# Performance work log

Measured on AMD Instinct MI355X. Metric: run time of the kernel, lower is better.

## Reference

```python
import jax, jax.numpy as jnp
import numpy as np

LN_EPS = 1e-5  # torch LayerNorm default
EPSILON = 1e-8  # slot attention epsilon


def layer_norm(x, g, b):
    mu = jnp.mean(x, axis=-1, keepdims=True)
    var = jnp.var(x, axis=-1, keepdims=True)
    return (x - mu) * jax.lax.rsqrt(var + LN_EPS) * g + b


def setup_inputs() -> dict:
    key = jax.random.key(0)
    ks = jax.random.split(key, 12)
    B, N, S, D, M = 64, 4096, 8, 256, 1024
    s = 0.02
    return {
        "features": jax.random.normal(ks[0], (B, N, D), jnp.float32),
        "slots_init": jax.random.normal(ks[1], (B, S, D), jnp.float32),
        # LayerNorm params (feature, slots, mlp)
        "g_feat": jnp.ones((D,), jnp.float32), "b_feat": jnp.zeros((D,), jnp.float32),
        "g_slots": jnp.ones((D,), jnp.float32), "b_slots": jnp.zeros((D,), jnp.float32),
        "g_mlp": jnp.ones((D,), jnp.float32), "b_mlp": jnp.zeros((D,), jnp.float32),
        # k/v/q projections (torch Linear weight: [out,in], no bias)
        "Wk": jax.random.normal(ks[2], (D, D), jnp.float32) * s,
        "Wv": jax.random.normal(ks[3], (D, D), jnp.float32) * s,
        "Wq": jax.random.normal(ks[4], (D, D), jnp.float32) * s,
        # GRUCell params: weight_ih/hh [3D, D] (gate order r, z, n), biases [3D]
        "w_ih": jax.random.normal(ks[5], (3 * D, D), jnp.float32) * s,
        "w_hh": jax.random.normal(ks[6], (3 * D, D), jnp.float32) * s,
        "b_ih": jnp.zeros((3 * D,), jnp.float32),
        "b_hh": jnp.zeros((3 * D,), jnp.float32),
        # MLP: Linear(D->M), ReLU, Linear(M->D)
        "W1": jax.random.normal(ks[7], (M, D), jnp.float32) * s,
        "b1": jnp.zeros((M,), jnp.float32),
        "W2": jax.random.normal(ks[8], (D, M), jnp.float32) * s,
        "b2": jnp.zeros((D,), jnp.float32),
        "num_iter": 3,
    }


def gru_cell(x, h, w_ih, w_hh, b_ih, b_hh):
    # x, h: [B*, D]; torch.nn.GRUCell math, gate order r, z, n
    gi = x @ w_ih.T + b_ih  # [B*, 3D]
    gh = h @ w_hh.T + b_hh
    i_r, i_z, i_n = jnp.split(gi, 3, axis=-1)
    h_r, h_z, h_n = jnp.split(gh, 3, axis=-1)
    r = jax.nn.sigmoid(i_r + h_r)
    z = jax.nn.sigmoid(i_z + h_z)
    n = jnp.tanh(i_n + r * h_n)
    return (1.0 - z) * n + z * h


def reference(features, slots_init, g_feat, b_feat, g_slots, b_slots, g_mlp, b_mlp,
              Wk, Wv, Wq, w_ih, w_hh, b_ih, b_hh, W1, b1, W2, b2, num_iter):
    feats = layer_norm(features, g_feat, b_feat)          # [B, N, D]
    k = feats @ Wk.T                                      # [B, N, D]
    v = feats @ Wv.T                                      # [B, N, D]
    B, N, D = v.shape
    scale = D ** -0.5
    slots = slots_init                                    # [B, S, D]
    S = slots.shape[1]
    attn = None
    for _ in range(num_iter):
        slots_prev = slots
        q = layer_norm(slots, g_slots, b_slots) @ Wq.T    # [B, S, D]
        attn_logits = jnp.einsum('bid,bjd->bij', q, k) * scale  # [B, S, N]
        attn = jax.nn.softmax(attn_logits, axis=1)        # softmax over slots
        attn = attn + EPSILON
        attn_wm = attn / jnp.sum(attn, axis=-1, keepdims=True)
        updates = jnp.einsum('bij,bjd->bid', attn_wm, v)  # [B, S, D]
        slots = gru_cell(updates.reshape(-1, D), slots_prev.reshape(-1, D),
                         w_ih, w_hh, b_ih, b_hh).reshape(B, S, D)
        h = jax.nn.relu(layer_norm(slots, g_mlp, b_mlp) @ W1.T + b1)
        slots = slots + h @ W2.T + b2
    return slots, attn
```

## Files before the change

### kernel.cpp

```cpp
#include <hip/hip_runtime.h>
#include <stdint.h>

typedef unsigned short u16;
typedef unsigned int u32;
typedef __bf16 bf16_t;
typedef bf16_t bf16x8 __attribute__((ext_vector_type(8)));
typedef float f32x4 __attribute__((ext_vector_type(4)));

#define DEV static __device__ __forceinline__

DEV float bf2f(u16 a) {
  union { u32 u; float f; } c; c.u = ((u32)a) << 16; return c.f;
}
DEV u16 f2bf(float f) {
  union { float f; u32 u; } c; c.f = f;
  return (u16)((c.u + 0x7FFFu + ((c.u >> 16) & 1u)) >> 16);
}
DEV f32x4 mfma16(bf16x8 a, bf16x8 b, f32x4 c) {
  return __builtin_amdgcn_mfma_f32_16x16x32_bf16(a, b, c, 0, 0, 0);
}
DEV float wave_sum(float v) {
#pragma unroll
  for (int off = 32; off > 0; off >>= 1) v += __shfl_xor(v, off, 64);
  return v;
}
DEV float sum16(float v) {
  v += __shfl_xor(v, 1, 64);
  v += __shfl_xor(v, 2, 64);
  v += __shfl_xor(v, 4, 64);
  v += __shfl_xor(v, 8, 64);
  return v;
}

__global__ void __launch_bounds__(256) init_prep(
    const float* __restrict__ Wk, const float* __restrict__ Wv,
    const float* __restrict__ gfeat, const float* __restrict__ bfeat,
    const float* __restrict__ slots_init,
    const float* __restrict__ Wq, const float* __restrict__ w_ih,
    const float* __restrict__ w_hh, const float* __restrict__ W1,
    const float* __restrict__ W2,
    u16* __restrict__ wkvp, float* __restrict__ ckv, float* __restrict__ dkv,
    float* __restrict__ slots,
    u16* __restrict__ wqb, u16* __restrict__ wihb, u16* __restrict__ whhb,
    u16* __restrict__ w1b, u16* __restrict__ w2b) {
  const int blk = blockIdx.x;
  const int tid = threadIdx.x;
  if (blk < 128) {
    const int o = blk * 4 + (tid >> 6);
    const int lane = tid & 63;
    const int d = lane * 4;
    const float* wrow = (o < 256) ? (Wk + (size_t)o * 256) : (Wv + (size_t)(o - 256) * 256);
    float4 w4 = *(const float4*)(wrow + d);
    float4 g4 = *(const float4*)(gfeat + d);
    float4 b4 = *(const float4*)(bfeat + d);
    float w[4] = {w4.x, w4.y, w4.z, w4.w};
    float g[4] = {g4.x, g4.y, g4.z, g4.w};
    float b[4] = {b4.x, b4.y, b4.z, b4.w};
    float cs = 0.f, ds = 0.f;
    u16 outp[4];
#pragma unroll
    for (int j = 0; j < 4; j++) {
      float wg = w[j] * g[j];
      cs += wg;
      ds += b[j] * w[j];
      outp[j] = f2bf(wg);
    }
    *(ushort4*)(wkvp + (size_t)o * 256 + d) = make_ushort4(outp[0], outp[1], outp[2], outp[3]);
    cs = wave_sum(cs);
    ds = wave_sum(ds);
    if (lane == 0) { ckv[o] = cs; dkv[o] = ds; }
  } else if (blk < 256) {
    const int idx = (blk - 128) * 1024 + tid * 4;
    *(float4*)(slots + idx) = *(const float4*)(slots_init + idx);
  } else {
    const int i = (blk - 256) * 1024 + tid * 4;
    const float* src; u16* dst; int off;
    if (i < 65536)       { src = Wq;   dst = wqb;  off = i; }
    else if (i < 262144) { src = w_ih; dst = wihb; off = i - 65536; }
    else if (i < 458752) { src = w_hh; dst = whhb; off = i - 262144; }
    else if (i < 720896) { src = W1;   dst = w1b;  off = i - 458752; }
    else                 { src = W2;   dst = w2b;  off = i - 720896; }
    float4 v = *(const float4*)(src + off);
    *(ushort4*)(dst + off) = make_ushort4(f2bf(v.x), f2bf(v.y), f2bf(v.z), f2bf(v.w));
  }
}

__global__ void __launch_bounds__(256, 2) gemm_kv(
    const float* __restrict__ feat, const u16* __restrict__ wkvp,
    const float* __restrict__ ckv, const float* __restrict__ dkv,
    u16* __restrict__ kbuf, u16* __restrict__ vtbuf) {
  __shared__ u16 Asm[128 * 256];
  __shared__ float mus[128];
  __shared__ float rss[128];
  const int tid = threadIdx.x;
  const int lane = tid & 63;
  const int wv = tid >> 6;
  const int cl = lane & 15;
  const int rq = lane >> 4;
  const int M0 = blockIdx.x * 128;
  const int wm = (wv & 1) * 64;
  const int wn = (wv >> 1) * 64;

#pragma unroll 4
  for (int i = 0; i < 16; i++) {
    const int gr = i * 256 + tid;
    const int m = gr >> 5;
    const int kc = gr & 31;
    const float* fp = feat + (size_t)(M0 + m) * 256 + kc * 8;
    float4 a0 = *(const float4*)fp;
    float4 a1 = *(const float4*)(fp + 4);
    float t1 = a0.x + a0.y + a0.z + a0.w + a1.x + a1.y + a1.z + a1.w;
    float t2 = a0.x * a0.x + a0.y * a0.y + a0.z * a0.z + a0.w * a0.w +
               a1.x * a1.x + a1.y * a1.y + a1.z * a1.z + a1.w * a1.w;
    t1 += __shfl_xor(t1, 1, 64);  t2 += __shfl_xor(t2, 1, 64);
    t1 += __shfl_xor(t1, 2, 64);  t2 += __shfl_xor(t2, 2, 64);
    t1 += __shfl_xor(t1, 4, 64);  t2 += __shfl_xor(t2, 4, 64);
    t1 += __shfl_xor(t1, 8, 64);  t2 += __shfl_xor(t2, 8, 64);
    t1 += __shfl_xor(t1, 16, 64); t2 += __shfl_xor(t2, 16, 64);
    if ((lane & 31) == 0) {
      float mu = t1 * (1.f / 256.f);
      float var = t2 * (1.f / 256.f) - mu * mu;
      mus[m] = mu;
      rss[m] = rsqrtf(var + 1e-5f);
    }
    u32 p0 = (u32)f2bf(a0.x) | ((u32)f2bf(a0.y) << 16);
    u32 p1 = (u32)f2bf(a0.z) | ((u32)f2bf(a0.w) << 16);
    u32 p2 = (u32)f2bf(a1.x) | ((u32)f2bf(a1.y) << 16);
    u32 p3 = (u32)f2bf(a1.z) | ((u32)f2bf(a1.w) << 16);
    const int sw = (kc & 24) | ((kc & 7) ^ (m & 7));
    *(uint4*)&Asm[m * 256 + sw * 8] = make_uint4(p0, p1, p2, p3);
  }
  __syncthreads();

  const f32x4 Z = {0.f, 0.f, 0.f, 0.f};
  const int b = M0 >> 12;
  const int col = cl;
  const int rq4 = rq * 4;

  for (int oc = 0; oc < 4; oc++) {
    const int O0 = oc * 128;
    f32x4 acc[4][4];
#pragma unroll
    for (int i = 0; i < 4; i++)
#pragma unroll
      for (int j = 0; j < 4; j++) acc[i][j] = Z;

#pragma unroll 2
    for (int kc8 = 0; kc8 < 8; kc8++) {
      bf16x8 af[4], bfr[4];
      const int c = kc8 * 4 + rq;
#pragma unroll
      for (int t = 0; t < 4; t++) {
        const int m = wm + t * 16 + cl;
        const int ca = (c & 24) | ((c & 7) ^ (m & 7));
        af[t] = *(const bf16x8*)&Asm[m * 256 + ca * 8];
        const int o = O0 + wn + t * 16 + cl;
        bfr[t] = *(const bf16x8*)(wkvp + (size_t)o * 256 + kc8 * 32 + rq * 8);
      }
#pragma unroll
      for (int i = 0; i < 4; i++)
#pragma unroll
        for (int j = 0; j < 4; j++) acc[i][j] = mfma16(af[i], bfr[j], acc[i][j]);
    }

    if (O0 < 256) {
#pragma unroll
      for (int i = 0; i < 4; i++) {
        const int mb = M0 + wm + i * 16 + rq4;
        const int ml = wm + i * 16 + rq4;
        float mu0[4], rs0[4];
#pragma unroll
        for (int r = 0; r < 4; r++) { mu0[r] = mus[ml + r]; rs0[r] = rss[ml + r]; }
#pragma unroll
        for (int j = 0; j < 4; j++) {
          const int o = O0 + wn + j * 16 + col;
          const float ck = ckv[o], dk = dkv[o];
#pragma unroll
          for (int r = 0; r < 4; r++) {
            float val = rs0[r] * acc[i][j][r] - rs0[r] * mu0[r] * ck + dk;
            kbuf[(size_t)(mb + r) * 256 + o] = f2bf(val);
          }
        }
      }
    } else {
#pragma unroll
      for (int i = 0; i < 4; i++) {
        const int mb = M0 + wm + i * 16 + rq4;
        const int ml = wm + i * 16 + rq4;
        const int n = mb & 4095;
        float mu0[4], rs0[4];
#pragma unroll
        for (int r = 0; r < 4; r++) { mu0[r] = mus[ml + r]; rs0[r] = rss[ml + r]; }
#pragma unroll
        for (int j = 0; j < 4; j++) {
          const int ov = O0 - 256 + wn + j * 16 + col;
          const float ck = ckv[ov + 256], dk = dkv[ov + 256];
          u16 t0 = f2bf(rs0[0] * acc[i][j][0] - rs0[0] * mu0[0] * ck + dk);
          u16 t1 = f2bf(rs0[1] * acc[i][j][1] - rs0[1] * mu0[1] * ck + dk);
          u16 t2 = f2bf(rs0[2] * acc[i][j][2] - rs0[2] * mu0[2] * ck + dk);
          u16 t3 = f2bf(rs0[3] * acc[i][j][3] - rs0[3] * mu0[3] * ck + dk);
          *(ushort4*)(vtbuf + (size_t)(b * 256 + ov) * 4096 + n) = make_ushort4(t0, t1, t2, t3);
        }
      }
    }
  }
}

__global__ void __launch_bounds__(256) attn_pass(
    const float* __restrict__ slots, const float* __restrict__ gs, const float* __restrict__ bs,
    const u16* __restrict__ wqb,
    const u16* __restrict__ kbuf, const u16* __restrict__ vtbuf,
    float* __restrict__ part_acc, float* __restrict__ part_den,
    float* __restrict__ attn_out, int store_attn) {
  __shared__ u16 pt[16 * 264];
  __shared__ u16 qld[16 * 264];
  const int chunk = blockIdx.x;
  const int b = blockIdx.y;
  const int n0 = chunk * 256;
  const int tid = threadIdx.x;
  const int lane = tid & 63;
  const int wv = tid >> 6;
  const int cl = lane & 15;
  const int rq = lane >> 4;
  const f32x4 Z = {0.f, 0.f, 0.f, 0.f};

  for (int i = tid; i < 8 * 264; i += 256) pt[8 * 264 + i] = 0;
  for (int rr = 0; rr < 2; rr++) {
    const int s = wv * 2 + rr;
    float4 x4 = *(const float4*)(slots + ((size_t)b * 8 + s) * 256 + lane * 4);
    float x[4] = {x4.x, x4.y, x4.z, x4.w};
    float s1 = x[0] + x[1] + x[2] + x[3];
    float s2 = x[0] * x[0] + x[1] * x[1] + x[2] * x[2] + x[3] * x[3];
    s1 = wave_sum(s1);
    s2 = wave_sum(s2);
    float mu = s1 * (1.f / 256.f);
    float rstd = rsqrtf(s2 * (1.f / 256.f) - mu * mu + 1e-5f);
    float4 g4 = *(const float4*)(gs + lane * 4);
    float4 b4 = *(const float4*)(bs + lane * 4);
    u16 o4[4];
    o4[0] = f2bf((x[0] - mu) * rstd * g4.x + b4.x);
    o4[1] = f2bf((x[1] - mu) * rstd * g4.y + b4.y);
    o4[2] = f2bf((x[2] - mu) * rstd * g4.z + b4.z);
    o4[3] = f2bf((x[3] - mu) * rstd * g4.w + b4.w);
    *(ushort4*)&pt[s * 264 + lane * 4] = make_ushort4(o4[0], o4[1], o4[2], o4[3]);
  }
  __syncthreads();

  {
    bf16x8 af[8];
#pragma unroll
    for (int ks = 0; ks < 8; ks++)
      af[ks] = *(const bf16x8*)&pt[cl * 264 + ks * 32 + rq * 8];
#pragma unroll
    for (int t = 0; t < 4; t++) {
      const int of = wv * 64 + t * 16;
      f32x4 acc = Z;
#pragma unroll
      for (int ks = 0; ks < 8; ks++) {
        bf16x8 bw = *(const bf16x8*)(wqb + (size_t)(of + cl) * 256 + ks * 32 + rq * 8);
        acc = mfma16(af[ks], bw, acc);
      }
#pragma unroll
      for (int r = 0; r < 4; r++)
        qld[(rq * 4 + r) * 264 + of + cl] = f2bf(acc[r]);
    }
  }
  __syncthreads();

  bf16x8 aq[8];
#pragma unroll
  for (int ks = 0; ks < 8; ks++)
    aq[ks] = *(const bf16x8*)&qld[cl * 264 + ks * 32 + rq * 8];

  float dacc[4] = {0.f, 0.f, 0.f, 0.f};
#pragma unroll
  for (int t = 0; t < 4; t++) {
    const int nl = (wv * 4 + t) * 16;
    f32x4 acc = Z;
    const int n = n0 + nl + cl;
#pragma unroll
    for (int ks = 0; ks < 8; ks++) {
      bf16x8 bk = *(const bf16x8*)(kbuf + ((size_t)b * 4096 + n) * 256 + ks * 32 + rq * 8);
      acc = mfma16(aq[ks], bk, acc);
    }
    float l[4];
#pragma unroll
    for (int r = 0; r < 4; r++) l[r] = acc[r] * 0.0625f;
    float m4 = fmaxf(fmaxf(l[0], l[1]), fmaxf(l[2], l[3]));
    float m8 = fmaxf(m4, __shfl_xor(m4, 16, 64));
    float e[4];
    float s4 = 0.f;
#pragma unroll
    for (int r = 0; r < 4; r++) { e[r] = __expf(l[r] - m8); s4 += e[r]; }
    float s8 = s4 + __shfl_xor(s4, 16, 64);
    float inv = 1.f / s8;
    float pa[4];
#pragma unroll
    for (int r = 0; r < 4; r++) pa[r] = e[r] * inv + 1e-8f;
#pragma unroll
    for (int r = 0; r < 4; r++) pt[(rq * 4 + r) * 264 + nl + cl] = f2bf(pa[r]);
    if (store_attn && lane < 32) {
#pragma unroll
      for (int r = 0; r < 4; r++)
        attn_out[((size_t)b * 8 + rq * 4 + r) * 4096 + n0 + nl + cl] = pa[r];
    }
#pragma unroll
    for (int r = 0; r < 4; r++) dacc[r] += sum16(pa[r]);
  }
  if (cl == 0 && lane < 32) {
#pragma unroll
    for (int r = 0; r < 4; r++)
      part_den[(((size_t)b * 16 + chunk) * 4 + wv) * 8 + rq * 4 + r] = dacc[r];
  }
  __syncthreads();

  bf16x8 ap[8];
#pragma unroll
  for (int ks = 0; ks < 8; ks++)
    ap[ks] = *(const bf16x8*)&pt[cl * 264 + ks * 32 + rq * 8];
#pragma unroll
  for (int t = 0; t < 4; t++) {
    const int df = wv * 64 + t * 16;
    f32x4 acc = Z;
    const int d = df + cl;
#pragma unroll
    for (int ks = 0; ks < 8; ks++) {
      bf16x8 bv = *(const bf16x8*)(vtbuf + ((size_t)b * 256 + d) * 4096 + n0 + ks * 32 + rq * 8);
      acc = mfma16(ap[ks], bv, acc);
    }
    if (lane < 32) {
#pragma unroll
      for (int r = 0; r < 4; r++)
        part_acc[(((size_t)b * 16 + chunk) * 8 + rq * 4 + r) * 256 + d] = acc[r];
    }
  }
}

__global__ void __launch_bounds__(256) slot_update(
    const float* __restrict__ part_acc, const float* __restrict__ part_den,
    float* __restrict__ slots,
    const u16* __restrict__ wihb, const u16* __restrict__ whhb,
    const float* __restrict__ b_ih, const float* __restrict__ b_hh,
    const float* __restrict__ gm, const float* __restrict__ bm,
    const u16* __restrict__ w1b, const float* __restrict__ b1,
    const u16* __restrict__ w2b, const float* __restrict__ b2,
    float* __restrict__ slots_out, int last) {
  __shared__ u16 ubf[16 * 264];
  __shared__ u16 hbf[16 * 264];
  __shared__ float hf32[8 * 256];
  __shared__ float midf[8 * 256];
  __shared__ u16 h1bf[16 * 1032];
  __shared__ float denl[8];
  const int b = blockIdx.x;
  const int tid = threadIdx.x;
  const int lane = tid & 63;
  const int wv = tid >> 6;
  const int cl = lane & 15;
  const int rq = lane >> 4;
  const f32x4 Z = {0.f, 0.f, 0.f, 0.f};

  for (int i = tid; i < 8 * 264; i += 256) { ubf[8 * 264 + i] = 0; hbf[8 * 264 + i] = 0; }
  if (tid < 8) {
    float s = 0.f;
    for (int c = 0; c < 64; c++) s += part_den[((size_t)b * 64 + c) * 8 + tid];
    denl[tid] = s;
  }
  __syncthreads();

#pragma unroll
  for (int i = 0; i < 8; i++) {
    float s = 0.f;
#pragma unroll
    for (int c = 0; c < 16; c++)
      s += part_acc[(((size_t)b * 16 + c) * 8 + i) * 256 + tid];
    float u = s / denl[i];
    ubf[i * 264 + tid] = f2bf(u);
    float h = slots[((size_t)b * 8 + i) * 256 + tid];
    hf32[i * 256 + tid] = h;
    hbf[i * 264 + tid] = f2bf(h);
  }
  __syncthreads();

  bf16x8 au[8], ah[8];
#pragma unroll
  for (int ks = 0; ks < 8; ks++) {
    au[ks] = *(const bf16x8*)&ubf[cl * 264 + ks * 32 + rq * 8];
    ah[ks] = *(const bf16x8*)&hbf[cl * 264 + ks * 32 + rq * 8];
  }
#pragma unroll
  for (int j4 = 0; j4 < 4; j4++) {
    const int j = wv * 4 + j4;
    f32x4 a_ir = Z, a_iz = Z, a_in = Z, a_hr = Z, a_hz = Z, a_hn = Z;
#pragma unroll
    for (int ks = 0; ks < 8; ks++) {
      const int koff = ks * 32 + rq * 8;
      const int o_r = j * 16 + cl;
      bf16x8 bri = *(const bf16x8*)(wihb + (size_t)o_r * 256 + koff);
      bf16x8 bzi = *(const bf16x8*)(wihb + (size_t)(256 + o_r) * 256 + koff);
      bf16x8 bni = *(const bf16x8*)(wihb + (size_t)(512 + o_r) * 256 + koff);
      bf16x8 brh = *(const bf16x8*)(whhb + (size_t)o_r * 256 + koff);
      bf16x8 bzh = *(const bf16x8*)(whhb + (size_t)(256 + o_r) * 256 + koff);
      bf16x8 bnh = *(const bf16x8*)(whhb + (size_t)(512 + o_r) * 256 + koff);
      a_ir = mfma16(au[ks], bri, a_ir);
      a_iz = mfma16(au[ks], bzi, a_iz);
      a_in = mfma16(au[ks], bni, a_in);
      a_hr = mfma16(ah[ks], brh, a_hr);
      a_hz = mfma16(ah[ks], bzh, a_hz);
      a_hn = mfma16(ah[ks], bnh, a_hn);
    }
    if (lane < 32) {
      const int d = j * 16 + cl;
      const float bihr = b_ih[d], bihz = b_ih[256 + d], bihn = b_ih[512 + d];
      const float bhhr = b_hh[d], bhhz = b_hh[256 + d], bhhn = b_hh[512 + d];
#pragma unroll
      for (int r = 0; r < 4; r++) {
        const int s = rq * 4 + r;
        float ir = a_ir[r] + bihr, iz = a_iz[r] + bihz, inn = a_in[r] + bihn;
        float hr = a_hr[r] + bhhr, hz = a_hz[r] + bhhz, hn = a_hn[r] + bhhn;
        float rg = 1.f / (1.f + __expf(-(ir + hr)));
        float zg = 1.f / (1.f + __expf(-(iz + hz)));
        float ng = tanhf(inn + rg * hn);
        float h = hf32[s * 256 + d];
        midf[s * 256 + d] = (1.f - zg) * ng + zg * h;
      }
    }
  }
  __syncthreads();

  for (int rr = 0; rr < 2; rr++) {
    const int s = wv * 2 + rr;
    float4 x4 = *(const float4*)&midf[s * 256 + lane * 4];
    float x[4] = {x4.x, x4.y, x4.z, x4.w};
    float s1 = x[0] + x[1] + x[2] + x[3];
    float s2 = x[0] * x[0] + x[1] * x[1] + x[2] * x[2] + x[3] * x[3];
    s1 = wave_sum(s1);
    s2 = wave_sum(s2);
    float mu = s1 * (1.f / 256.f);
    float rstd = rsqrtf(s2 * (1.f / 256.f) - mu * mu + 1e-5f);
    float4 g4 = *(const float4*)(gm + lane * 4);
    float4 b4 = *(const float4*)(bm + lane * 4);
    u16 o4[4];
    o4[0] = f2bf((x[0] - mu) * rstd * g4.x + b4.x);
    o4[1] = f2bf((x[1] - mu) * rstd * g4.y + b4.y);
    o4[2] = f2bf((x[2] - mu) * rstd * g4.z + b4.z);
    o4[3] = f2bf((x[3] - mu) * rstd * g4.w + b4.w);
    *(ushort4*)&ubf[s * 264 + lane * 4] = make_ushort4(o4[0], o4[1], o4[2], o4[3]);
  }
  __syncthreads();

  bf16x8 al[8];
#pragma unroll
  for (int ks = 0; ks < 8; ks++)
    al[ks] = *(const bf16x8*)&ubf[cl * 264 + ks * 32 + rq * 8];
#pragma unroll
  for (int t = 0; t < 16; t++) {
    const int of = wv * 256 + t * 16;
    f32x4 acc = Z;
#pragma unroll
    for (int ks = 0; ks < 8; ks++) {
      bf16x8 bw = *(const bf16x8*)(w1b + (size_t)(of + cl) * 256 + ks * 32 + rq * 8);
      acc = mfma16(al[ks], bw, acc);
    }
    const float bb = b1[of + cl];
#pragma unroll
    for (int r = 0; r < 4; r++)
      h1bf[(rq * 4 + r) * 1032 + of + cl] = f2bf(fmaxf(acc[r] + bb, 0.f));
  }
  __syncthreads();

  f32x4 acc2[4] = {Z, Z, Z, Z};
  for (int ks = 0; ks < 32; ks++) {
    bf16x8 ah1 = *(const bf16x8*)&h1bf[cl * 1032 + ks * 32 + rq * 8];
#pragma unroll
    for (int t = 0; t < 4; t++) {
      const int o = wv * 64 + t * 16 + cl;
      bf16x8 bw = *(const bf16x8*)(w2b + (size_t)o * 1024 + ks * 32 + rq * 8);
      acc2[t] = mfma16(ah1, bw, acc2[t]);
    }
  }
  if (lane < 32) {
#pragma unroll
    for (int t = 0; t < 4; t++) {
      const int o = wv * 64 + t * 16 + cl;
      const float bb = b2[o];
#pragma unroll
      for (int r = 0; r < 4; r++) {
        const int s = rq * 4 + r;
        float val = midf[s * 256 + o] + acc2[t][r] + bb;
        slots[((size_t)b * 8 + s) * 256 + o] = val;
        if (last) slots_out[((size_t)b * 8 + s) * 256 + o] = val;
      }
    }
  }
}

extern "C" void kernel_launch(void* const* d_in, const int* in_sizes, int n_in,
                              void* d_out, int out_size, void* d_ws, size_t ws_size,
                              hipStream_t stream) {
  (void)in_sizes; (void)n_in; (void)out_size;
  const float* features = (const float*)d_in[0];
  const float* slots_init = (const float*)d_in[1];
  const float* g_feat = (const float*)d_in[2];
  const float* b_feat = (const float*)d_in[3];
  const float* g_slots = (const float*)d_in[4];
  const float* b_slots = (const float*)d_in[5];
  const float* g_mlp = (const float*)d_in[6];
  const float* b_mlp = (const float*)d_in[7];
  const float* Wk = (const float*)d_in[8];
  const float* Wv = (const float*)d_in[9];
  const float* Wq = (const float*)d_in[10];
  const float* w_ih = (const float*)d_in[11];
  const float* w_hh = (const float*)d_in[12];
  const float* b_ih = (const float*)d_in[13];
  const float* b_hh = (const float*)d_in[14];
  const float* W1 = (const float*)d_in[15];
  const float* b1 = (const float*)d_in[16];
  const float* W2 = (const float*)d_in[17];
  const float* b2 = (const float*)d_in[18];

  const size_t REQUIRED = 280236032ull;
  if (ws_size < REQUIRED) return;

  char* ws = (char*)d_ws;
  u16* kbuf = (u16*)(ws + 0);
  u16* vtbuf = (u16*)(ws + 134217728);
  float* part_acc = (float*)(ws + 268959744);
  float* part_den = (float*)(ws + 277348352);
  float* slots = (float*)(ws + 277479424);
  u16* wkvp = (u16*)(ws + 278003712);
  float* ckv = (float*)(ws + 278265856);
  float* dkv = (float*)(ws + 278267904);
  u16* wqb = (u16*)(ws + 278269952);
  u16* wihb = (u16*)(ws + 278401024);
  u16* whhb = (u16*)(ws + 278794240);
  u16* w1b = (u16*)(ws + 279187456);
  u16* w2b = (u16*)(ws + 279711744);

  float* out_slots = (float*)d_out;
  float* out_attn = out_slots + 131072;

  init_prep<<<1216, 256, 0, stream>>>(Wk, Wv, g_feat, b_feat, slots_init, Wq, w_ih, w_hh, W1, W2,
                                      wkvp, ckv, dkv, slots, wqb, wihb, whhb, w1b, w2b);
  gemm_kv<<<2048, 256, 0, stream>>>(features, wkvp, ckv, dkv, kbuf, vtbuf);
  for (int it = 0; it < 3; it++) {
    attn_pass<<<dim3(16, 64), 256, 0, stream>>>(slots, g_slots, b_slots, wqb, kbuf, vtbuf,
                                                part_acc, part_den, out_attn, it == 2 ? 1 : 0);
    slot_update<<<64, 256, 0, stream>>>(part_acc, part_den, slots, wihb, whhb, b_ih, b_hh,
                                        g_mlp, b_mlp, w1b, b1, w2b, b2, out_slots, it == 2 ? 1 : 0);
  }
}
```

Baseline: 943.0 us.

## Fold Wk into query and Wv into slot update instead of projecting features

Drops the big K/V projection GEMM over all B*N features. Only the normalized features are stored, row-major and transposed, in bf16. The query is multiplied by Wk (q·Wk) inside attn_pass so logits are taken directly against the normalized features. Wv is applied after aggregation in slot_update, since attn·(F Wv^T) = (attn·F) Wv^T. This removes a large matmul and its reads and writes, but adds small per-iteration GEMMs and changes bf16 rounding points.

```diff
diff --git a/kernel.cpp b/kernel.cpp
--- a/kernel.cpp
+++ b/kernel.cpp
@@ -34,75 +34,70 @@
 
 __global__ void __launch_bounds__(256) init_prep(
     const float* __restrict__ Wk, const float* __restrict__ Wv,
-    const float* __restrict__ gfeat, const float* __restrict__ bfeat,
     const float* __restrict__ slots_init,
     const float* __restrict__ Wq, const float* __restrict__ w_ih,
     const float* __restrict__ w_hh, const float* __restrict__ W1,
     const float* __restrict__ W2,
-    u16* __restrict__ wkvp, float* __restrict__ ckv, float* __restrict__ dkv,
     float* __restrict__ slots,
     u16* __restrict__ wqb, u16* __restrict__ wihb, u16* __restrict__ whhb,
-    u16* __restrict__ w1b, u16* __restrict__ w2b) {
+    u16* __restrict__ w1b, u16* __restrict__ w2b,
+    u16* __restrict__ wvb, u16* __restrict__ wktb) {
   const int blk = blockIdx.x;
   const int tid = threadIdx.x;
   if (blk < 128) {
-    const int o = blk * 4 + (tid >> 6);
-    const int lane = tid & 63;
-    const int d = lane * 4;
-    const float* wrow = (o < 256) ? (Wk + (size_t)o * 256) : (Wv + (size_t)(o - 256) * 256);
-    float4 w4 = *(const float4*)(wrow + d);
-    float4 g4 = *(const float4*)(gfeat + d);
-    float4 b4 = *(const float4*)(bfeat + d);
-    float w[4] = {w4.x, w4.y, w4.z, w4.w};
-    float g[4] = {g4.x, g4.y, g4.z, g4.w};
-    float b[4] = {b4.x, b4.y, b4.z, b4.w};
-    float cs = 0.f, ds = 0.f;
-    u16 outp[4];
-#pragma unroll
-    for (int j = 0; j < 4; j++) {
-      float wg = w[j] * g[j];
-      cs += wg;
-      ds += b[j] * w[j];
-      outp[j] = f2bf(wg);
-    }
-    *(ushort4*)(wkvp + (size_t)o * 256 + d) = make_ushort4(outp[0], outp[1], outp[2], outp[3]);
-    cs = wave_sum(cs);
-    ds = wave_sum(ds);
-    if (lane == 0) { ckv[o] = cs; dkv[o] = ds; }
-  } else if (blk < 256) {
-    const int idx = (blk - 128) * 1024 + tid * 4;
+    const int idx = blk * 1024 + tid * 4;
     *(float4*)(slots + idx) = *(const float4*)(slots_init + idx);
-  } else {
-    const int i = (blk - 256) * 1024 + tid * 4;
+  } else if (blk < 1152) {
+    const int i = (blk - 128) * 1024 + tid * 4;
     const float* src; u16* dst; int off;
     if (i < 65536)       { src = Wq;   dst = wqb;  off = i; }
     else if (i < 262144) { src = w_ih; dst = wihb; off = i - 65536; }
     else if (i < 458752) { src = w_hh; dst = whhb; off = i - 262144; }
     else if (i < 720896) { src = W1;   dst = w1b;  off = i - 458752; }
-    else                 { src = W2;   dst = w2b;  off = i - 720896; }
+    else if (i < 983040) { src = W2;   dst = w2b;  off = i - 720896; }
+    else                 { src = Wv;   dst = wvb;  off = i - 983040; }
     float4 v = *(const float4*)(src + off);
     *(ushort4*)(dst + off) = make_ushort4(f2bf(v.x), f2bf(v.y), f2bf(v.z), f2bf(v.w));
-  }
-}
-
-__global__ void __launch_bounds__(256, 2) gemm_kv(
-    const float* __restrict__ feat, const u16* __restrict__ wkvp,
-    const float* __restrict__ ckv, const float* __restrict__ dkv,
-    u16* __restrict__ kbuf, u16* __restrict__ vtbuf) {
-  __shared__ u16 Asm[128 * 256];
-  __shared__ float mus[128];
-  __shared__ float rss[128];
+  } else {
+    __shared__ u16 tl[64][66];
+    const int tb = blk - 1152;
+    const int r0 = (tb >> 2) * 64;
+    const int c0 = (tb & 3) * 64;
+    const int r = tid >> 2;
+    const int cseg = (tid & 3) * 16;
+#pragma unroll
+    for (int q = 0; q < 4; q++) {
+      float4 v = *(const float4*)(Wk + (size_t)(r0 + r) * 256 + c0 + cseg + q * 4);
+      tl[r][cseg + q * 4 + 0] = f2bf(v.x);
+      tl[r][cseg + q * 4 + 1] = f2bf(v.y);
+      tl[r][cseg + q * 4 + 2] = f2bf(v.z);
+      tl[r][cseg + q * 4 + 3] = f2bf(v.w);
+    }
+    __syncthreads();
+    const int c = tid >> 2;
+    const int rseg = (tid & 3) * 16;
+    u16 out[16];
+#pragma unroll
+    for (int j = 0; j < 16; j++) out[j] = tl[rseg + j][c];
+#pragma unroll
+    for (int q = 0; q < 4; q++)
+      *(ushort4*)(wktb + (size_t)(c0 + c) * 256 + r0 + rseg + q * 4) =
+          make_ushort4(out[q * 4], out[q * 4 + 1], out[q * 4 + 2], out[q * 4 + 3]);
+  }
+}
+
+__global__ void __launch_bounds__(256) ln_feat(
+    const float* __restrict__ feat, const float* __restrict__ g,
+    const float* __restrict__ bia,
+    u16* __restrict__ fbuf, u16* __restrict__ fbuf_t) {
+  __shared__ u16 T[64 * 264];
   const int tid = threadIdx.x;
-  const int lane = tid & 63;
-  const int wv = tid >> 6;
-  const int cl = lane & 15;
-  const int rq = lane >> 4;
-  const int M0 = blockIdx.x * 128;
-  const int wm = (wv & 1) * 64;
-  const int wn = (wv >> 1) * 64;
-
-#pragma unroll 4
-  for (int i = 0; i < 16; i++) {
+  const int M0 = blockIdx.x * 64;
+  const int b = M0 >> 12;
+  const int nb = M0 & 4095;
+
+#pragma unroll 2
+  for (int i = 0; i < 8; i++) {
     const int gr = i * 256 + tid;
     const int m = gr >> 5;
     const int kc = gr & 31;
@@ -117,99 +112,45 @@
     t1 += __shfl_xor(t1, 4, 64);  t2 += __shfl_xor(t2, 4, 64);
     t1 += __shfl_xor(t1, 8, 64);  t2 += __shfl_xor(t2, 8, 64);
     t1 += __shfl_xor(t1, 16, 64); t2 += __shfl_xor(t2, 16, 64);
-    if ((lane & 31) == 0) {
-      float mu = t1 * (1.f / 256.f);
-      float var = t2 * (1.f / 256.f) - mu * mu;
-      mus[m] = mu;
-      rss[m] = rsqrtf(var + 1e-5f);
-    }
-    u32 p0 = (u32)f2bf(a0.x) | ((u32)f2bf(a0.y) << 16);
-    u32 p1 = (u32)f2bf(a0.z) | ((u32)f2bf(a0.w) << 16);
-    u32 p2 = (u32)f2bf(a1.x) | ((u32)f2bf(a1.y) << 16);
-    u32 p3 = (u32)f2bf(a1.z) | ((u32)f2bf(a1.w) << 16);
-    const int sw = (kc & 24) | ((kc & 7) ^ (m & 7));
-    *(uint4*)&Asm[m * 256 + sw * 8] = make_uint4(p0, p1, p2, p3);
-  }
-  __syncthreads();
-
-  const f32x4 Z = {0.f, 0.f, 0.f, 0.f};
-  const int b = M0 >> 12;
-  const int col = cl;
-  const int rq4 = rq * 4;
-
-  for (int oc = 0; oc < 4; oc++) {
-    const int O0 = oc * 128;
-    f32x4 acc[4][4];
-#pragma unroll
-    for (int i = 0; i < 4; i++)
-#pragma unroll
-      for (int j = 0; j < 4; j++) acc[i][j] = Z;
-
-#pragma unroll 2
-    for (int kc8 = 0; kc8 < 8; kc8++) {
-      bf16x8 af[4], bfr[4];
-      const int c = kc8 * 4 + rq;
-#pragma unroll
-      for (int t = 0; t < 4; t++) {
-        const int m = wm + t * 16 + cl;
-        const int ca = (c & 24) | ((c & 7) ^ (m & 7));
-        af[t] = *(const bf16x8*)&Asm[m * 256 + ca * 8];
-        const int o = O0 + wn + t * 16 + cl;
-        bfr[t] = *(const bf16x8*)(wkvp + (size_t)o * 256 + kc8 * 32 + rq * 8);
-      }
-#pragma unroll
-      for (int i = 0; i < 4; i++)
-#pragma unroll
-        for (int j = 0; j < 4; j++) acc[i][j] = mfma16(af[i], bfr[j], acc[i][j]);
-    }
-
-    if (O0 < 256) {
-#pragma unroll
-      for (int i = 0; i < 4; i++) {
-        const int mb = M0 + wm + i * 16 + rq4;
-        const int ml = wm + i * 16 + rq4;
-        float mu0[4], rs0[4];
-#pragma unroll
-        for (int r = 0; r < 4; r++) { mu0[r] = mus[ml + r]; rs0[r] = rss[ml + r]; }
-#pragma unroll
-        for (int j = 0; j < 4; j++) {
-          const int o = O0 + wn + j * 16 + col;
-          const float ck = ckv[o], dk = dkv[o];
-#pragma unroll
-          for (int r = 0; r < 4; r++) {
-            float val = rs0[r] * acc[i][j][r] - rs0[r] * mu0[r] * ck + dk;
-            kbuf[(size_t)(mb + r) * 256 + o] = f2bf(val);
-          }
-        }
-      }
-    } else {
-#pragma unroll
-      for (int i = 0; i < 4; i++) {
-        const int mb = M0 + wm + i * 16 + rq4;
-        const int ml = wm + i * 16 + rq4;
-        const int n = mb & 4095;
-        float mu0[4], rs0[4];
-#pragma unroll
-        for (int r = 0; r < 4; r++) { mu0[r] = mus[ml + r]; rs0[r] = rss[ml + r]; }
-#pragma unroll
-        for (int j = 0; j < 4; j++) {
-          const int ov = O0 - 256 + wn + j * 16 + col;
-          const float ck = ckv[ov + 256], dk = dkv[ov + 256];
-          u16 t0 = f2bf(rs0[0] * acc[i][j][0] - rs0[0] * mu0[0] * ck + dk);
-          u16 t1 = f2bf(rs0[1] * acc[i][j][1] - rs0[1] * mu0[1] * ck + dk);
-          u16 t2 = f2bf(rs0[2] * acc[i][j][2] - rs0[2] * mu0[2] * ck + dk);
-          u16 t3 = f2bf(rs0[3] * acc[i][j][3] - rs0[3] * mu0[3] * ck + dk);
-          *(ushort4*)(vtbuf + (size_t)(b * 256 + ov) * 4096 + n) = make_ushort4(t0, t1, t2, t3);
-        }
-      }
-    }
+    const float mu = t1 * (1.f / 256.f);
+    const float rs = rsqrtf(t2 * (1.f / 256.f) - mu * mu + 1e-5f);
+    float4 g0 = *(const float4*)(g + kc * 8);
+    float4 g1 = *(const float4*)(g + kc * 8 + 4);
+    float4 b0 = *(const float4*)(bia + kc * 8);
+    float4 b1 = *(const float4*)(bia + kc * 8 + 4);
+    u16 y[8];
+    y[0] = f2bf((a0.x - mu) * rs * g0.x + b0.x);
+    y[1] = f2bf((a0.y - mu) * rs * g0.y + b0.y);
+    y[2] = f2bf((a0.z - mu) * rs * g0.z + b0.z);
+    y[3] = f2bf((a0.w - mu) * rs * g0.w + b0.w);
+    y[4] = f2bf((a1.x - mu) * rs * g1.x + b1.x);
+    y[5] = f2bf((a1.y - mu) * rs * g1.y + b1.y);
+    y[6] = f2bf((a1.z - mu) * rs * g1.z + b1.z);
+    y[7] = f2bf((a1.w - mu) * rs * g1.w + b1.w);
+    uint4 pk = make_uint4((u32)y[0] | ((u32)y[1] << 16), (u32)y[2] | ((u32)y[3] << 16),
+                          (u32)y[4] | ((u32)y[5] << 16), (u32)y[6] | ((u32)y[7] << 16));
+    *(uint4*)&T[m * 264 + kc * 8] = pk;
+    *(uint4*)(fbuf + (size_t)(M0 + m) * 256 + kc * 8) = pk;
+  }
+  __syncthreads();
+
+  const int dl = tid >> 4;
+  const int ns4 = (tid & 15) * 4;
+#pragma unroll 4
+  for (int o = 0; o < 16; o++) {
+    const int d = dl + o * 16;
+    u16 v0 = T[(ns4 + 0) * 264 + d];
+    u16 v1 = T[(ns4 + 1) * 264 + d];
+    u16 v2 = T[(ns4 + 2) * 264 + d];
+    u16 v3 = T[(ns4 + 3) * 264 + d];
+    *(ushort4*)(fbuf_t + ((size_t)b * 256 + d) * 4096 + nb + ns4) = make_ushort4(v0, v1, v2, v3);
   }
 }
 
 __global__ void __launch_bounds__(256) attn_pass(
     const float* __restrict__ slots, const float* __restrict__ gs, const float* __restrict__ bs,
-    const u16* __restrict__ wqb,
-    const u16* __restrict__ kbuf, const u16* __restrict__ vtbuf,
+    const u16* __restrict__ wqb, const u16* __restrict__ wktb,
+    const u16* __restrict__ fbuf, const u16* __restrict__ fbuf_t,
     float* __restrict__ part_acc, float* __restrict__ part_den,
     float* __restrict__ attn_out, int store_attn) {
   __shared__ u16 pt[16 * 264];
@@ -267,10 +208,31 @@
   }
   __syncthreads();
 
+  {
+    bf16x8 a2[8];
+#pragma unroll
+    for (int ks = 0; ks < 8; ks++)
+      a2[ks] = *(const bf16x8*)&qld[cl * 264 + ks * 32 + rq * 8];
+#pragma unroll
+    for (int t = 0; t < 4; t++) {
+      const int of = wv * 64 + t * 16;
+      f32x4 acc = Z;
+#pragma unroll
+      for (int ks = 0; ks < 8; ks++) {
+        bf16x8 bw = *(const bf16x8*)(wktb + (size_t)(of + cl) * 256 + ks * 32 + rq * 8);
+        acc = mfma16(a2[ks], bw, acc);
+      }
+#pragma unroll
+      for (int r = 0; r < 4; r++)
+        pt[(rq * 4 + r) * 264 + of + cl] = f2bf(acc[r]);
+    }
+  }
+  __syncthreads();
+
   bf16x8 aq[8];
 #pragma unroll
   for (int ks = 0; ks < 8; ks++)
-    aq[ks] = *(const bf16x8*)&qld[cl * 264 + ks * 32 + rq * 8];
+    aq[ks] = *(const bf16x8*)&pt[cl * 264 + ks * 32 + rq * 8];
 
   float dacc[4] = {0.f, 0.f, 0.f, 0.f};
 #pragma unroll
@@ -280,7 +242,7 @@
     const int n = n0 + nl + cl;
 #pragma unroll
     for (int ks = 0; ks < 8; ks++) {
-      bf16x8 bk = *(const bf16x8*)(kbuf + ((size_t)b * 4096 + n) * 256 + ks * 32 + rq * 8);
+      bf16x8 bk = *(const bf16x8*)(fbuf + ((size_t)b * 4096 + n) * 256 + ks * 32 + rq * 8);
       acc = mfma16(aq[ks], bk, acc);
     }
     float l[4];
@@ -298,7 +260,7 @@
 #pragma unroll
     for (int r = 0; r < 4; r++) pa[r] = e[r] * inv + 1e-8f;
 #pragma unroll
-    for (int r = 0; r < 4; r++) pt[(rq * 4 + r) * 264 + nl + cl] = f2bf(pa[r]);
+    for (int r = 0; r < 4; r++) qld[(rq * 4 + r) * 264 + nl + cl] = f2bf(pa[r]);
     if (store_attn && lane < 32) {
 #pragma unroll
       for (int r = 0; r < 4; r++)
@@ -317,7 +279,7 @@
   bf16x8 ap[8];
 #pragma unroll
   for (int ks = 0; ks < 8; ks++)
-    ap[ks] = *(const bf16x8*)&pt[cl * 264 + ks * 32 + rq * 8];
+    ap[ks] = *(const bf16x8*)&qld[cl * 264 + ks * 32 + rq * 8];
 #pragma unroll
   for (int t = 0; t < 4; t++) {
     const int df = wv * 64 + t * 16;
@@ -325,7 +287,7 @@
     const int d = df + cl;
 #pragma unroll
     for (int ks = 0; ks < 8; ks++) {
-      bf16x8 bv = *(const bf16x8*)(vtbuf + ((size_t)b * 256 + d) * 4096 + n0 + ks * 32 + rq * 8);
+      bf16x8 bv = *(const bf16x8*)(fbuf_t + ((size_t)b * 256 + d) * 4096 + n0 + ks * 32 + rq * 8);
       acc = mfma16(ap[ks], bv, acc);
     }
     if (lane < 32) {
@@ -344,9 +306,11 @@
     const float* __restrict__ gm, const float* __restrict__ bm,
     const u16* __restrict__ w1b, const float* __restrict__ b1,
     const u16* __restrict__ w2b, const float* __restrict__ b2,
+    const u16* __restrict__ wvb,
     float* __restrict__ slots_out, int last) {
   __shared__ u16 ubf[16 * 264];
   __shared__ u16 hbf[16 * 264];
+  __shared__ u16 updbf[16 * 264];
   __shared__ float hf32[8 * 256];
   __shared__ float midf[8 * 256];
   __shared__ u16 h1bf[16 * 1032];
@@ -381,10 +345,31 @@
   }
   __syncthreads();
 
+  {
+    bf16x8 apf[8];
+#pragma unroll
+    for (int ks = 0; ks < 8; ks++)
+      apf[ks] = *(const bf16x8*)&ubf[cl * 264 + ks * 32 + rq * 8];
+#pragma unroll
+    for (int t = 0; t < 4; t++) {
+      const int of = wv * 64 + t * 16;
+      f32x4 acc = Z;
+#pragma unroll
+      for (int ks = 0; ks < 8; ks++) {
+        bf16x8 bw = *(const bf16x8*)(wvb + (size_t)(of + cl) * 256 + ks * 32 + rq * 8);
+        acc = mfma16(apf[ks], bw, acc);
+      }
+#pragma unroll
+      for (int r = 0; r < 4; r++)
+        updbf[(rq * 4 + r) * 264 + of + cl] = f2bf(acc[r]);
+    }
+  }
+  __syncthreads();
+
   bf16x8 au[8], ah[8];
 #pragma unroll
   for (int ks = 0; ks < 8; ks++) {
-    au[ks] = *(const bf16x8*)&ubf[cl * 264 + ks * 32 + rq * 8];
+    au[ks] = *(const bf16x8*)&updbf[cl * 264 + ks * 32 + rq * 8];
     ah[ks] = *(const bf16x8*)&hbf[cl * 264 + ks * 32 + rq * 8];
   }
 #pragma unroll
@@ -522,14 +507,13 @@
   if (ws_size < REQUIRED) return;
 
   char* ws = (char*)d_ws;
-  u16* kbuf = (u16*)(ws + 0);
-  u16* vtbuf = (u16*)(ws + 134217728);
+  u16* fbuf = (u16*)(ws + 0);
+  u16* fbuf_t = (u16*)(ws + 134217728);
   float* part_acc = (float*)(ws + 268959744);
   float* part_den = (float*)(ws + 277348352);
   float* slots = (float*)(ws + 277479424);
-  u16* wkvp = (u16*)(ws + 278003712);
-  float* ckv = (float*)(ws + 278265856);
-  float* dkv = (float*)(ws + 278267904);
+  u16* wktb = (u16*)(ws + 278003712);
+  u16* wvb = (u16*)(ws + 278134784);
   u16* wqb = (u16*)(ws + 278269952);
   u16* wihb = (u16*)(ws + 278401024);
   u16* whhb = (u16*)(ws + 278794240);
@@ -539,13 +523,15 @@
   float* out_slots = (float*)d_out;
   float* out_attn = out_slots + 131072;
 
-  init_prep<<<1216, 256, 0, stream>>>(Wk, Wv, g_feat, b_feat, slots_init, Wq, w_ih, w_hh, W1, W2,
-                                      wkvp, ckv, dkv, slots, wqb, wihb, whhb, w1b, w2b);
-  gemm_kv<<<2048, 256, 0, stream>>>(features, wkvp, ckv, dkv, kbuf, vtbuf);
+  init_prep<<<1168, 256, 0, stream>>>(Wk, Wv, slots_init, Wq, w_ih, w_hh, W1, W2,
+                                      slots, wqb, wihb, whhb, w1b, w2b, wvb, wktb);
+  ln_feat<<<4096, 256, 0, stream>>>(features, g_feat, b_feat, fbuf, fbuf_t);
   for (int it = 0; it < 3; it++) {
-    attn_pass<<<dim3(16, 64), 256, 0, stream>>>(slots, g_slots, b_slots, wqb, kbuf, vtbuf,
-                                                part_acc, part_den, out_attn, it == 2 ? 1 : 0);
+    attn_pass<<<dim3(16, 64), 256, 0, stream>>>(slots, g_slots, b_slots, wqb, wktb,
+                                                fbuf, fbuf_t, part_acc, part_den,
+                                                out_attn, it == 2 ? 1 : 0);
     slot_update<<<64, 256, 0, stream>>>(part_acc, part_den, slots, wihb, whhb, b_ih, b_hh,
-                                        g_mlp, b_mlp, w1b, b1, w2b, b2, out_slots, it == 2 ? 1 : 0);
-  }
-}
+                                        g_mlp, b_mlp, w1b, b1, w2b, b2, wvb,
+                                        out_slots, it == 2 ? 1 : 0);
+  }
+}
```

New measurement: 891.4 us. 5.5% less time.
